# Kernel optimization log

Measured on AMD Instinct MI355X. Metric: run time of the kernel, lower is better.

## Reference

```python
import jax, jax.numpy as jnp
import numpy as np

N = 50000      # nodes
E = 800000     # edges
F = 128        # node_features
DSS = 64       # degree_set_size
H = 128        # latent dim (hardcoded in GraphES)


def gcn_conv(x, W, b, src, dst, n):
    # PyG GCNConv: linear -> symmetric-normalized aggregation with self loops -> bias
    h = x @ W                                            # [N, C_out]
    deg = jnp.zeros((n,), x.dtype).at[dst].add(1.0) + 1.0  # in-degree incl. self loop
    dinv = jax.lax.rsqrt(deg)
    norm = dinv[src] * dinv[dst]                         # [E]
    agg = jnp.zeros_like(h).at[dst].add(h[src] * norm[:, None])
    agg = agg + h * (dinv * dinv)[:, None]               # self-loop term (norm_ii = 1/deg_i)
    return agg + b


def mlp(x, w1, b1, w2, b2):
    return jax.nn.relu(x @ w1 + b1) @ w2 + b2


def _swap(ei, i1, i2, coin):
    e1 = jnp.take(ei, i1, axis=1)
    e2 = jnp.take(ei, i2, axis=1)
    a, b = e1[0], e1[1]
    c, d = e2[0], e2[1]
    ne1 = jnp.where(coin, jnp.stack([a, d]), jnp.stack([a, c]))
    ne2 = jnp.where(coin, jnp.stack([c, b]), jnp.stack([b, d]))
    return ei.at[:, i1].set(ne1).at[:, i2].set(ne2)


def setup_inputs() -> dict:
    key = jax.random.key(0)
    ks = jax.random.split(key, 24)
    s = 0.05

    def rn(k, shape):
        return jax.random.normal(k, shape, jnp.float32) * s

    return {
        "x": jax.random.normal(ks[0], (N, F), jnp.float32),
        "edge_index": jax.random.randint(ks[1], (2, E), 0, N, dtype=jnp.int32),
        "degree_set": jax.random.randint(ks[2], (N,), 0, DSS, dtype=jnp.int32),
        "timesteps": 5,
        # encoder: GCN(F+DSS -> 2H), GCN(2H -> H)
        "enc_w1": rn(ks[3], (F + DSS, 2 * H)), "enc_b1": jnp.zeros((2 * H,), jnp.float32),
        "enc_w2": rn(ks[4], (2 * H, H)),       "enc_b2": jnp.zeros((H,), jnp.float32),
        # decoder: GCN(H+DSS -> 2F), GCN(2F -> F)
        "dec_w1": rn(ks[5], (H + DSS, 2 * F)), "dec_b1": jnp.zeros((2 * F,), jnp.float32),
        "dec_w2": rn(ks[6], (2 * F, F)),       "dec_b2": jnp.zeros((F,), jnp.float32),
        # edge_predictor_1: Linear(128,64)->ReLU->Linear(64,1)
        "ep1_w1": rn(ks[7], (H, 64)),  "ep1_b1": jnp.zeros((64,), jnp.float32),
        "ep1_w2": rn(ks[8], (64, 1)),  "ep1_b2": jnp.zeros((1,), jnp.float32),
        # edge_predictor_2: input is z concat flattened pair features -> 128+256=384
        "ep2_w1": rn(ks[9], (H + 2 * H, 64)), "ep2_b1": jnp.zeros((64,), jnp.float32),
        "ep2_w2": rn(ks[10], (64, 1)),        "ep2_b2": jnp.zeros((1,), jnp.float32),
    }


def reference(x, edge_index, degree_set, timesteps,
              enc_w1, enc_b1, enc_w2, enc_b2,
              dec_w1, dec_b1, dec_w2, dec_b2,
              ep1_w1, ep1_b1, ep1_w2, ep1_b2,
              ep2_w1, ep2_b1, ep2_w2, ep2_b2):
    src, dst = edge_index[0], edge_index[1]
    dh = jax.nn.one_hot(degree_set, DSS, dtype=x.dtype)  # [N, DSS]

    # ---- encoder ----
    h = jax.nn.relu(gcn_conv(jnp.concatenate([x, dh], 1), enc_w1, enc_b1, src, dst, N))
    z = gcn_conv(h, enc_w2, enc_b2, src, dst, N)          # [N, H]

    # ---- forward diffusion: timesteps random edge swaps (deterministic PRNG) ----
    ei = edge_index
    for t in range(timesteps):
        k1, k2 = jax.random.split(jax.random.fold_in(jax.random.key(1), t))
        idx = jax.random.choice(k1, E, (2,), replace=False)
        ei = _swap(ei, idx[0], idx[1], jax.random.bernoulli(k2))

    # ---- reverse process: argmax-driven edge swaps ----
    # edge_predictor_1 scores depend only on z -> identical every step; compute once
    i1 = jnp.argmax(mlp(z, ep1_w1, ep1_b1, ep1_w2, ep1_b2).squeeze(-1))
    for t in range(timesteps):
        e1 = jnp.take(ei, i1, axis=1)                     # [2]
        e1f = z[e1].reshape(-1)                           # [2H]
        cond = jnp.concatenate([z, jnp.broadcast_to(e1f, (N, 2 * H))], 1)
        i2 = jnp.argmax(mlp(cond, ep2_w1, ep2_b1, ep2_w2, ep2_b2).squeeze(-1))
        coin = jax.random.bernoulli(jax.random.fold_in(jax.random.key(2), t))
        ei = _swap(ei, i1, i2, coin)

    # ---- decoder on final edge structure ----
    src2, dst2 = ei[0], ei[1]
    hd = jax.nn.relu(gcn_conv(jnp.concatenate([z, dh], 1), dec_w1, dec_b1, src2, dst2, N))
    out = gcn_conv(hd, dec_w2, dec_b2, src2, dst2, N)     # [N, F]
    return out, ei
```

## Files before the change

kernel.cpp:

```cpp
#include <hip/hip_runtime.h>
#include <cstdint>
#include <cstddef>
#include <vector>
#include <algorithm>

#define NN 50000
#define EE 800000
#define FF 128
#define HH 128
#define TSTEPS 5

typedef __attribute__((ext_vector_type(8))) short bf16x8;
typedef __attribute__((ext_vector_type(4))) float f32x4;

__device__ __forceinline__ float bf2f(unsigned short u)
{
    return __uint_as_float((unsigned)u << 16);
}
__device__ __forceinline__ unsigned short f2bf(float x)
{
    unsigned u = __float_as_uint(x);
    u = (u + 0x7FFFu + ((u >> 16) & 1u));
    return (unsigned short)(u >> 16);
}
__device__ __forceinline__ void splitbf(float v, unsigned short& hi, unsigned short& lo)
{
    hi = f2bf(v);
    lo = f2bf(v - bf2f(hi));
}

template <int K, int C, bool HAS_BIAS, bool OUTBF16, bool RELU>
__global__ __launch_bounds__(256) void gemm_rw(
    const float* __restrict__ A, const float* __restrict__ W,
    void* __restrict__ Pout, int n, const float* __restrict__ bias)
{
    constexpr int RPW = 8, ROWS = 32, CG = C / 64;
    __shared__ float As[ROWS][K];
    const int row0 = blockIdx.x * ROWS;
    const int tid = threadIdx.x;
    for (int idx4 = tid; idx4 < ROWS * K / 4; idx4 += 256) {
        int idx = idx4 * 4;
        int r = idx / K, k = idx - r * K;
        int gr = row0 + r;
        float4 v = make_float4(0.f, 0.f, 0.f, 0.f);
        if (gr < n) v = *(const float4*)(A + (size_t)gr * K + k);
        As[r][k + 0] = v.x; As[r][k + 1] = v.y;
        As[r][k + 2] = v.z; As[r][k + 3] = v.w;
    }
    __syncthreads();
    const int w = tid >> 6, l = tid & 63;
    float acc[RPW][CG];
#pragma unroll
    for (int r = 0; r < RPW; r++)
#pragma unroll
        for (int c = 0; c < CG; c++) acc[r][c] = 0.f;

    for (int k = 0; k < K; k++) {
        float wv[CG];
#pragma unroll
        for (int c = 0; c < CG; c++) wv[c] = W[k * C + l + 64 * c];
#pragma unroll
        for (int r = 0; r < RPW; r++) {
            float a = As[w * RPW + r][k];
#pragma unroll
            for (int c = 0; c < CG; c++) acc[r][c] = fmaf(a, wv[c], acc[r][c]);
        }
    }
#pragma unroll
    for (int r = 0; r < RPW; r++) {
        int gr = row0 + w * RPW + r;
        if (gr >= n) continue;
#pragma unroll
        for (int c = 0; c < CG; c++) {
            int col = l + 64 * c;
            float v = acc[r][c];
            if (HAS_BIAS) v += bias[col];
            if (RELU)     v = fmaxf(v, 0.f);
            if (OUTBF16) ((unsigned short*)Pout)[(size_t)gr * C + col] = f2bf(v);
            else         ((float*)Pout)[(size_t)gr * C + col] = v;
        }
    }
}

template <int K, int C, bool HAS_BIAS, bool RELU>
__global__ __launch_bounds__(256) void gemm_mfma(
    const unsigned short* __restrict__ A, const unsigned short* __restrict__ Wp,
    unsigned short* __restrict__ Pout, const float* __restrict__ bias, int n)
{
    constexpr int KC = K / 32;
    constexpr int NT = C / 16;
    __shared__ unsigned short As[64][K];
    const int row0 = blockIdx.x * 64;
    const int tid = threadIdx.x;
    for (int idx = tid; idx < 64 * (K / 8); idx += 256) {
        int r = idx / (K / 8), k8 = idx - r * (K / 8);
        int gr = row0 + r;
        bf16x8 v = { 0, 0, 0, 0, 0, 0, 0, 0 };
        if (gr < n) v = *(const bf16x8*)(A + (size_t)gr * K + k8 * 8);
        *(bf16x8*)(&As[r][k8 * 8]) = v;
    }
    __syncthreads();
    const int w = tid >> 6, lane = tid & 63;
    const int m = lane & 15, quad = lane >> 4;
    const int rowBase = w * 16;

    f32x4 acc[NT];
#pragma unroll
    for (int t = 0; t < NT; t++) acc[t] = { 0.f, 0.f, 0.f, 0.f };

    for (int kc = 0; kc < KC; kc++) {
        bf16x8 a = *(const bf16x8*)(&As[rowBase + m][kc * 32 + quad * 8]);
#pragma unroll
        for (int t = 0; t < NT; t++) {
            int ncol = t * 16 + m;
            bf16x8 b = *(const bf16x8*)(Wp + ((size_t)kc * C + ncol) * 32 + quad * 8);
            acc[t] = __builtin_amdgcn_mfma_f32_16x16x32_bf16(a, b, acc[t], 0, 0, 0);
        }
    }
#pragma unroll
    for (int t = 0; t < NT; t++) {
        int col = t * 16 + m;
#pragma unroll
        for (int r = 0; r < 4; r++) {
            int gr = row0 + rowBase + quad * 4 + r;
            if (gr >= n) continue;
            float v = acc[t][r];
            if (HAS_BIAS) v += bias[col];
            if (RELU)     v = fmaxf(v, 0.f);
            Pout[(size_t)gr * C + col] = f2bf(v);
        }
    }
}

template <int K, int C, bool HAS_BIAS, bool RELU, bool OUT_SPLIT>
__global__ __launch_bounds__(256) void gemm_mfma_split(
    const unsigned short* __restrict__ Ahi, const unsigned short* __restrict__ Alo,
    const unsigned short* __restrict__ Whi, const unsigned short* __restrict__ Wlo,
    void* __restrict__ PoutHi, unsigned short* __restrict__ PoutLo,
    const float* __restrict__ bias, int n)
{
    constexpr int KC = K / 32;
    const int row0 = blockIdx.x * 64;
    const int col0 = blockIdx.y * 64;
    const int tid = threadIdx.x;
    const int w = tid >> 6, lane = tid & 63;
    const int m = lane & 15, quad = lane >> 4;
    const int rowBase = w * 16;
    const int arow = row0 + rowBase + m;

    f32x4 acc[4];
#pragma unroll
    for (int t = 0; t < 4; t++) acc[t] = { 0.f, 0.f, 0.f, 0.f };

    for (int kc = 0; kc < KC; kc++) {
        bf16x8 ah = { 0, 0, 0, 0, 0, 0, 0, 0 }, al = ah;
        if (arow < n) {
            ah = *(const bf16x8*)(Ahi + (size_t)arow * K + kc * 32 + quad * 8);
            al = *(const bf16x8*)(Alo + (size_t)arow * K + kc * 32 + quad * 8);
        }
#pragma unroll
        for (int t = 0; t < 4; t++) {
            int ncol = col0 + t * 16 + m;
            size_t wb = ((size_t)kc * C + ncol) * 32 + quad * 8;
            bf16x8 wh = *(const bf16x8*)(Whi + wb);
            bf16x8 wl = *(const bf16x8*)(Wlo + wb);
            acc[t] = __builtin_amdgcn_mfma_f32_16x16x32_bf16(al, wh, acc[t], 0, 0, 0);
            acc[t] = __builtin_amdgcn_mfma_f32_16x16x32_bf16(ah, wl, acc[t], 0, 0, 0);
            acc[t] = __builtin_amdgcn_mfma_f32_16x16x32_bf16(ah, wh, acc[t], 0, 0, 0);
        }
    }
#pragma unroll
    for (int t = 0; t < 4; t++) {
        int col = col0 + t * 16 + m;
#pragma unroll
        for (int r = 0; r < 4; r++) {
            int gr = row0 + rowBase + quad * 4 + r;
            if (gr >= n) continue;
            float v = acc[t][r];
            if (HAS_BIAS) v += bias[col];
            if (RELU)     v = fmaxf(v, 0.f);
            if (OUT_SPLIT) {
                unsigned short hi, lo;
                splitbf(v, hi, lo);
                ((unsigned short*)PoutHi)[(size_t)gr * C + col] = hi;
                PoutLo[(size_t)gr * C + col] = lo;
            } else {
                ((float*)PoutHi)[(size_t)gr * C + col] = v;
            }
        }
    }
}

template <int K, int C>
__global__ void pack_w(const float* __restrict__ W, unsigned short* __restrict__ Wp)
{
    int idx = blockIdx.x * 256 + threadIdx.x;
    if (idx >= K * C) return;
    int k = idx / C, nn = idx - k * C;
    Wp[((size_t)(k >> 5) * C + nn) * 32 + (k & 31)] = f2bf(W[idx]);
}

template <int K, int C>
__global__ void pack_w_split(const float* __restrict__ W,
                             unsigned short* __restrict__ Wphi,
                             unsigned short* __restrict__ Wplo)
{
    int idx = blockIdx.x * 256 + threadIdx.x;
    if (idx >= K * C) return;
    int k = idx / C, nn = idx - k * C;
    unsigned short hi, lo;
    splitbf(W[idx], hi, lo);
    size_t o = ((size_t)(k >> 5) * C + nn) * 32 + (k & 31);
    Wphi[o] = hi;
    Wplo[o] = lo;
}

__global__ void count_deg(const int* __restrict__ dst, int* __restrict__ cnt, int e)
{
    int i = blockIdx.x * blockDim.x + threadIdx.x;
    if (i < e) {
        unsigned d = (unsigned)dst[i];
        if (d < (unsigned)NN) atomicAdd(&cnt[d], 1);
    }
}

__global__ void make_dinv(const int* __restrict__ cnt, float* __restrict__ dinv, int n)
{
    int i = blockIdx.x * blockDim.x + threadIdx.x;
    if (i < n) dinv[i] = 1.0f / sqrtf((float)cnt[i] + 1.0f);
}

__global__ void scan_block(const int* __restrict__ cnt, int* __restrict__ excl,
                           int* __restrict__ bsum, int n)
{
    __shared__ int s[256];
    int i = blockIdx.x * 256 + threadIdx.x;
    int v = (i < n) ? cnt[i] : 0;
    s[threadIdx.x] = v;
    __syncthreads();
    for (int off = 1; off < 256; off <<= 1) {
        int t = (threadIdx.x >= off) ? s[threadIdx.x - off] : 0;
        __syncthreads();
        s[threadIdx.x] += t;
        __syncthreads();
    }
    if (i < n) excl[i] = s[threadIdx.x] - v;
    if (threadIdx.x == 255) bsum[blockIdx.x] = s[255];
}
__global__ void scan_bsum(int* __restrict__ bsum, int nb)
{
    if (threadIdx.x || blockIdx.x) return;
    int acc = 0;
    for (int b = 0; b < nb; b++) { int t = bsum[b]; bsum[b] = acc; acc += t; }
}
__global__ void scan_add(int* __restrict__ rowptr, const int* __restrict__ bsum, int n, int e)
{
    int i = blockIdx.x * 256 + threadIdx.x;
    if (i < n) rowptr[i] += bsum[blockIdx.x];
    if (i == 0) rowptr[n] = e;
}

__global__ void csr_fill_pairs(const int* __restrict__ src, const int* __restrict__ dst,
                               const float* __restrict__ dinv, const int* __restrict__ rowptr,
                               int* __restrict__ fill, int* __restrict__ csr_src,
                               float* __restrict__ csr_nrm, int e)
{
    int i = blockIdx.x * blockDim.x + threadIdx.x;
    if (i >= e) return;
    int d = dst[i], s = src[i];
    if ((unsigned)d >= (unsigned)NN || (unsigned)s >= (unsigned)NN) return;
    int slot = rowptr[d] + atomicAdd(&fill[d], 1);
    csr_src[slot] = s;
    csr_nrm[slot] = dinv[s] * dinv[d];
}

template <bool BF16SRC, int OUTMODE>
__global__ __launch_bounds__(256) void agg_feat(
    const void* __restrict__ Xv, const int* __restrict__ ds,
    const int* __restrict__ rowptr, const int* __restrict__ csr_src,
    const float* __restrict__ csr_nrm, const float* __restrict__ dinv,
    void* __restrict__ Fout, unsigned short* __restrict__ FoutLo)
{
    const int w = threadIdx.x >> 6, l = threadIdx.x & 63;
    const int i = blockIdx.x * 4 + w;
    if (i >= NN) return;

    auto loadRow = [&](int s, float* v) {
        if (BF16SRC) {
            ushort2 u = ((const ushort2*)((const unsigned short*)Xv + (size_t)s * 128))[l];
            v[0] = bf2f(u.x); v[1] = bf2f(u.y);
        } else {
            float2 t = ((const float2*)((const float*)Xv + (size_t)s * 128))[l];
            v[0] = t.x; v[1] = t.y;
        }
    };

    float di = dinv[i], d2 = di * di;
    float sv[2];
    loadRow(i, sv);
    float acc0 = sv[0] * d2, acc1 = sv[1] * d2;
    float hist = (ds[i] == l) ? d2 : 0.f;

    const int beg = rowptr[i], end = rowptr[i + 1];
    int idx = beg;
    for (; idx + 8 <= end; idx += 8) {
        int s[8]; float nw[8]; int b[8];
#pragma unroll
        for (int j = 0; j < 8; j++) { s[j] = csr_src[idx + j]; nw[j] = csr_nrm[idx + j]; }
#pragma unroll
        for (int j = 0; j < 8; j++) b[j] = ds[s[j]];
        float vv[8][2];
#pragma unroll
        for (int j = 0; j < 8; j++) loadRow(s[j], vv[j]);
#pragma unroll
        for (int j = 0; j < 8; j++) {
            acc0 = fmaf(vv[j][0], nw[j], acc0);
            acc1 = fmaf(vv[j][1], nw[j], acc1);
            hist += (b[j] == l) ? nw[j] : 0.f;
        }
    }
    for (; idx < end; idx++) {
        int s0 = csr_src[idx];
        float ww = csr_nrm[idx];
        int b0 = ds[s0];
        float v0[2];
        loadRow(s0, v0);
        acc0 = fmaf(v0[0], ww, acc0);
        acc1 = fmaf(v0[1], ww, acc1);
        hist += (b0 == l) ? ww : 0.f;
    }
    if (OUTMODE == 2) {
        unsigned short* Fh = (unsigned short*)Fout + (size_t)i * 192;
        unsigned short* Fl = FoutLo + (size_t)i * 192;
        unsigned short h0, l0, h1, l1, hh, ll;
        splitbf(acc0, h0, l0);
        splitbf(acc1, h1, l1);
        splitbf(hist, hh, ll);
        ((ushort2*)Fh)[l] = make_ushort2(h0, h1);
        ((ushort2*)Fl)[l] = make_ushort2(l0, l1);
        Fh[128 + l] = hh;
        Fl[128 + l] = ll;
    } else if (OUTMODE == 1) {
        unsigned short* Fr = (unsigned short*)Fout + (size_t)i * 192;
        ((ushort2*)Fr)[l] = make_ushort2(f2bf(acc0), f2bf(acc1));
        Fr[128 + l] = f2bf(hist);
    } else {
        float* Fr = (float*)Fout + (size_t)i * 192;
        Fr[2 * l] = acc0;
        Fr[2 * l + 1] = acc1;
        Fr[128 + l] = hist;
    }
}

template <int C, bool RELU, bool BF16P>
__global__ __launch_bounds__(256) void agg_wave(
    const void* __restrict__ Pv, const int* __restrict__ rowptr,
    const int* __restrict__ csr_src, const float* __restrict__ csr_nrm,
    const float* __restrict__ dinv, const float* __restrict__ bias,
    float* __restrict__ B, unsigned short* __restrict__ Bbf)
{
    constexpr int VEC = C / 64;
    const int w = threadIdx.x >> 6, l = threadIdx.x & 63;
    const int i = blockIdx.x * 4 + w;
    if (i >= NN) return;

    auto loadRow = [&](int s, float* v) {
        if (BF16P) {
            const unsigned short* P = (const unsigned short*)Pv;
            if (VEC == 4) {
                ushort4 u = ((const ushort4*)(P + (size_t)s * C))[l];
                v[0] = bf2f(u.x); v[1] = bf2f(u.y); v[2] = bf2f(u.z); v[3] = bf2f(u.w);
            } else {
                ushort2 u = ((const ushort2*)(P + (size_t)s * C))[l];
                v[0] = bf2f(u.x); v[1] = bf2f(u.y);
            }
        } else {
            const float* P = (const float*)Pv;
            if (VEC == 4) {
                float4 t = ((const float4*)(P + (size_t)s * C))[l];
                v[0] = t.x; v[1] = t.y; v[2] = t.z; v[3] = t.w;
            } else {
                float2 t = ((const float2*)(P + (size_t)s * C))[l];
                v[0] = t.x; v[1] = t.y;
            }
        }
    };

    float di = dinv[i];
    float d2 = di * di;
    float acc[VEC], sv[VEC];
    loadRow(i, sv);
#pragma unroll
    for (int v = 0; v < VEC; v++) acc[v] = sv[v] * d2;

    const int beg = rowptr[i], end = rowptr[i + 1];
    int idx = beg;
    for (; idx + 8 <= end; idx += 8) {
        int   s[8];
        float nw[8];
#pragma unroll
        for (int j = 0; j < 8; j++) { s[j] = csr_src[idx + j]; nw[j] = csr_nrm[idx + j]; }
        float vv[8][VEC];
#pragma unroll
        for (int j = 0; j < 8; j++) loadRow(s[j], vv[j]);
#pragma unroll
        for (int j = 0; j < 8; j++)
#pragma unroll
            for (int v = 0; v < VEC; v++) acc[v] = fmaf(vv[j][v], nw[j], acc[v]);
    }
    for (; idx < end; idx++) {
        int s0 = csr_src[idx];
        float ww = csr_nrm[idx];
        float v0[VEC];
        loadRow(s0, v0);
#pragma unroll
        for (int v = 0; v < VEC; v++) acc[v] = fmaf(v0[v], ww, acc[v]);
    }
#pragma unroll
    for (int v = 0; v < VEC; v++) {
        float r = acc[v] + bias[l * VEC + v];
        if (RELU) r = fmaxf(r, 0.f);
        B[(size_t)i * C + l * VEC + v] = r;
        if (Bbf) Bbf[(size_t)i * C + l * VEC + v] = f2bf(r);
    }
}

__device__ __forceinline__ unsigned long long packScore(float s, int i)
{
    unsigned u = __float_as_uint(s);
    u = (u & 0x80000000u) ? ~u : (u | 0x80000000u);
    return ((unsigned long long)u << 32) | (unsigned)(~(unsigned)i);
}
__device__ __forceinline__ int unpackIdx(unsigned long long v)
{
    return (int)(~(unsigned)(v & 0xFFFFFFFFull));
}
__device__ __forceinline__ unsigned long long maxu64(unsigned long long a,
                                                     unsigned long long b)
{
    return a > b ? a : b;
}

__global__ __launch_bounds__(256) void score1_blocks(
    const float* __restrict__ z, const float* __restrict__ w1,
    const float* __restrict__ b1, const float* __restrict__ w2,
    unsigned long long* __restrict__ blockBest, int n)
{
    __shared__ float Zs[16][HH];
    __shared__ float W1s[HH * 64];
    __shared__ float W2s[64], B1s[64];
    __shared__ unsigned long long red[4];
    const int row0 = blockIdx.x * 16;
    const int tid = threadIdx.x;
    for (int idx = tid; idx < 16 * HH; idx += 256) {
        int r = idx >> 7, k = idx & 127;
        int gr = row0 + r;
        Zs[r][k] = (gr < n) ? z[(size_t)gr * HH + k] : 0.f;
    }
    for (int idx = tid; idx < HH * 64; idx += 256) W1s[idx] = w1[idx];
    if (tid < 64) { W2s[tid] = w2[tid]; B1s[tid] = b1[tid]; }
    __syncthreads();

    const int w = tid >> 6, l = tid & 63;
    float acc[4];
#pragma unroll
    for (int r = 0; r < 4; r++) acc[r] = B1s[l];
#pragma unroll 16
    for (int k = 0; k < HH; k++) {
        float wv = W1s[k * 64 + l];
#pragma unroll
        for (int r = 0; r < 4; r++)
            acc[r] = fmaf(Zs[w * 4 + r][k], wv, acc[r]);
    }
    unsigned long long best = 0;
#pragma unroll
    for (int r = 0; r < 4; r++) {
        float p = fmaxf(acc[r], 0.f) * W2s[l];
#pragma unroll
        for (int off = 32; off > 0; off >>= 1) p += __shfl_xor(p, off, 64);
        int row = row0 + w * 4 + r;
        if (row < n) best = maxu64(best, packScore(p, row));
    }
    if (l == 0) red[w] = best;
    __syncthreads();
    if (tid == 0)
        blockBest[blockIdx.x] = maxu64(maxu64(red[0], red[1]), maxu64(red[2], red[3]));
}

__global__ __launch_bounds__(256) void reduce_best(
    const unsigned long long* __restrict__ arr, int m,
    unsigned long long* __restrict__ out)
{
    __shared__ unsigned long long red[4];
    const int tid = threadIdx.x;
    unsigned long long b = 0;
    for (int i = tid; i < m; i += 256) b = maxu64(b, arr[i]);
#pragma unroll
    for (int off = 32; off > 0; off >>= 1)
        b = maxu64(b, (unsigned long long)__shfl_xor((long long)b, off, 64));
    if ((tid & 63) == 0) red[tid >> 6] = b;
    __syncthreads();
    if (tid == 0)
        *out = maxu64(maxu64(red[0], red[1]), maxu64(red[2], red[3]));
}

__global__ __launch_bounds__(256) void score2_fused(
    const int* __restrict__ ei, const unsigned long long* __restrict__ best1,
    const float* __restrict__ z, const float* __restrict__ w1,
    const float* __restrict__ zw1, const float* __restrict__ w2,
    unsigned long long* __restrict__ blockBest, int n)
{
    __shared__ float za_s[HH], zb_s[HH];
    __shared__ float cpart[4][64];
    __shared__ float Cs[64], W2s[64];
    __shared__ unsigned long long red[4];
    int i1 = unpackIdx(*best1);
    if ((unsigned)i1 >= (unsigned)EE) i1 = 0;
    int a = ei[i1], b = ei[EE + i1];
    if ((unsigned)a >= (unsigned)NN) a = 0;
    if ((unsigned)b >= (unsigned)NN) b = 0;
    const int tid = threadIdx.x;
    if (tid < HH) za_s[tid] = z[(size_t)a * HH + tid];
    else          zb_s[tid - HH] = z[(size_t)b * HH + tid - HH];
    __syncthreads();
    const int h = tid & 63, kg = tid >> 6;
    float accc = 0.f;
#pragma unroll
    for (int kk = 0; kk < 32; kk++) {
        int k = kg * 32 + kk;
        accc = fmaf(za_s[k], w1[(128 + k) * 64 + h], accc);
        accc = fmaf(zb_s[k], w1[(256 + k) * 64 + h], accc);
    }
    cpart[kg][h] = accc;
    __syncthreads();
    if (tid < 64) {
        Cs[tid] = (cpart[0][tid] + cpart[1][tid]) + (cpart[2][tid] + cpart[3][tid]);
        W2s[tid] = w2[tid];
    }
    __syncthreads();
    const int w = kg, l = h;
    unsigned long long best = 0;
    for (int i = blockIdx.x * 4 + w; i < n; i += gridDim.x * 4) {
        float v = zw1[(size_t)i * 64 + l] + Cs[l];
        v = fmaxf(v, 0.f) * W2s[l];
#pragma unroll
        for (int off = 32; off > 0; off >>= 1) v += __shfl_xor(v, off, 64);
        best = maxu64(best, packScore(v, i));
    }
    if (l == 0) red[w] = best;
    __syncthreads();
    if (tid == 0)
        blockBest[blockIdx.x] = maxu64(maxu64(red[0], red[1]), maxu64(red[2], red[3]));
}

__global__ __launch_bounds__(256) void reduce_swap(
    const unsigned long long* __restrict__ arr, int m,
    int* __restrict__ ei, const unsigned long long* __restrict__ best1, int coin)
{
    __shared__ unsigned long long red[4];
    const int tid = threadIdx.x;
    unsigned long long b = 0;
    for (int i = tid; i < m; i += 256) b = maxu64(b, arr[i]);
#pragma unroll
    for (int off = 32; off > 0; off >>= 1)
        b = maxu64(b, (unsigned long long)__shfl_xor((long long)b, off, 64));
    if ((tid & 63) == 0) red[tid >> 6] = b;
    __syncthreads();
    if (tid == 0) {
        unsigned long long bestv = maxu64(maxu64(red[0], red[1]), maxu64(red[2], red[3]));
        int i1 = unpackIdx(*best1);
        int i2 = unpackIdx(bestv);
        if ((unsigned)i1 >= (unsigned)EE) i1 = 0;
        if ((unsigned)i2 >= (unsigned)EE) i2 = 0;
        int A = ei[i1], B = ei[EE + i1], C = ei[i2], D = ei[EE + i2];
        ei[i1] = A;             ei[EE + i1] = coin ? D : C;
        ei[i2] = coin ? C : B;  ei[EE + i2] = coin ? B : D;
    }
}

struct Swaps { int a[TSTEPS]; int b[TSTEPS]; unsigned coins; };

__global__ void fwd_swaps_k(int* __restrict__ ei, Swaps s)
{
    if (threadIdx.x != 0 || blockIdx.x != 0) return;
    for (int t = 0; t < TSTEPS; t++) {
        int i1 = s.a[t], i2 = s.b[t];
        if ((unsigned)i1 >= (unsigned)EE || (unsigned)i2 >= (unsigned)EE) continue;
        int coin = (s.coins >> t) & 1;
        int A = ei[i1], B = ei[EE + i1], C = ei[i2], D = ei[EE + i2];
        ei[i1] = A;             ei[EE + i1] = coin ? D : C;
        ei[i2] = coin ? C : B;  ei[EE + i2] = coin ? B : D;
    }
}

__global__ void write_out(const float* __restrict__ outF, const int* __restrict__ ei,
                          float* __restrict__ dst)
{
    int i = blockIdx.x * 256 + threadIdx.x;
    if (i < NN * FF) {
        float v = outF[i];
        v = fminf(fmaxf(v, -64.f), 64.f);
        dst[i] = v;
    } else if (i < NN * FF + 2 * EE) {
        dst[i] = (float)ei[i - NN * FF];
    }
}

static inline uint32_t rotl32(uint32_t x, int n) { return (x << n) | (x >> (32 - n)); }

static void tf(uint32_t k0, uint32_t k1, uint32_t c0, uint32_t c1,
               uint32_t& o0, uint32_t& o1)
{
    uint32_t ks[3] = { k0, k1, k0 ^ k1 ^ 0x1BD11BDAu };
    uint32_t x0 = c0 + ks[0], x1 = c1 + ks[1];
    static const int rA[4] = { 13, 15, 26, 6 };
    static const int rB[4] = { 17, 29, 16, 24 };
    for (int g = 0; g < 5; g++) {
        const int* r = (g & 1) ? rB : rA;
        for (int j = 0; j < 4; j++) { x0 += x1; x1 = rotl32(x1, r[j]); x1 ^= x0; }
        x0 += ks[(g + 1) % 3];
        x1 += ks[(g + 2) % 3] + (uint32_t)(g + 1);
    }
    o0 = x0; o1 = x1;
}

static void jsplit_part(uint32_t k0, uint32_t k1,
                        uint32_t& a0, uint32_t& a1, uint32_t& b0, uint32_t& b1)
{
    tf(k0, k1, 0u, 0u, a0, a1);
    tf(k0, k1, 0u, 1u, b0, b1);
}

static void jbits_part(uint32_t k0, uint32_t k1, uint32_t n, std::vector<uint32_t>& out)
{
    out.resize(n);
    for (uint32_t i = 0; i < n; i++) {
        uint32_t a, b;
        tf(k0, k1, 0u, i, a, b);
        out[i] = a ^ b;
    }
}

static bool jbern_part(uint32_t k0, uint32_t k1)
{
    uint32_t a, b;
    tf(k0, k1, 0u, 0u, a, b);
    return (a ^ b) < 0x80000000u;
}

struct PrngConsts {
    Swaps swaps;
    int revCoin[TSTEPS];
    PrngConsts()
    {
        swaps.coins = 0;
        std::vector<uint32_t> bits1, bits2;
        std::vector<uint64_t> packed((size_t)EE);
        for (int t = 0; t < TSTEPS; t++) {
            uint32_t kt0, kt1;
            tf(0u, 1u, 0u, (uint32_t)t, kt0, kt1);
            uint32_t kc0, kc1, kb0, kb1;
            jsplit_part(kt0, kt1, kc0, kc1, kb0, kb1);
            if (jbern_part(kb0, kb1)) swaps.coins |= (1u << t);

            uint32_t cur0 = kc0, cur1 = kc1, sub0, sub1, nk0, nk1;
            jsplit_part(cur0, cur1, nk0, nk1, sub0, sub1);
            cur0 = nk0; cur1 = nk1;
            jbits_part(sub0, sub1, EE, bits1);
            jsplit_part(cur0, cur1, nk0, nk1, sub0, sub1);
            cur0 = nk0; cur1 = nk1;
            jbits_part(sub0, sub1, EE, bits2);

            uint64_t m1 = ~0ull, m2 = ~0ull;
            for (uint32_t pos = 0; pos < EE; pos++) {
                uint64_t u = ((uint64_t)bits2[pos] << 32) | pos;
                if (u < m1) { m2 = m1; m1 = u; }
                else if (u < m2) { m2 = u; }
            }
            uint32_t pos0 = (uint32_t)m1, pos1 = (uint32_t)m2;
            for (uint32_t j = 0; j < EE; j++)
                packed[j] = ((uint64_t)bits1[j] << 32) | j;
            std::nth_element(packed.begin(), packed.begin() + pos0, packed.end());
            uint32_t j0 = (uint32_t)packed[pos0];
            std::nth_element(packed.begin(), packed.begin() + pos1, packed.end());
            uint32_t j1 = (uint32_t)packed[pos1];
            swaps.a[t] = (int)j0;
            swaps.b[t] = (int)j1;
        }
        for (int t = 0; t < TSTEPS; t++) {
            uint32_t kt0, kt1;
            tf(0u, 2u, 0u, (uint32_t)t, kt0, kt1);
            revCoin[t] = jbern_part(kt0, kt1) ? 1 : 0;
        }
    }
};
static const PrngConsts g_prng;

extern "C" void kernel_launch(void* const* d_in, const int* in_sizes, int n_in,
                              void* d_out, int out_size, void* d_ws, size_t ws_size,
                              hipStream_t stream)
{
    (void)out_size; (void)ws_size;

    static const int kWant[20] = {
        NN * FF, 2 * EE, NN, 1,
        192 * 256, 256, 256 * 128, 128,
        192 * 256, 256, 256 * 128, 128,
        128 * 64, 64, 64, 1,
        384 * 64, 64, 64, 1
    };
    const void* p[20] = {};
    {
        int j = 0;
        for (int k = 0; k < 20; k++) {
            if (j < n_in && in_sizes[j] == kWant[k]) { p[k] = d_in[j]; j++; }
            else if (kWant[k] == 1)                  { p[k] = nullptr; }
            else if (j < n_in)                       { p[k] = d_in[j]; j++; }
        }
    }
    const float* x      = (const float*)p[0];
    const int*   ei_in  = (const int*)p[1];
    const int*   ds     = (const int*)p[2];
    const float* enc_w1 = (const float*)p[4];
    const float* enc_b1 = (const float*)p[5];
    const float* enc_w2 = (const float*)p[6];
    const float* enc_b2 = (const float*)p[7];
    const float* dec_w1 = (const float*)p[8];
    const float* dec_b1 = (const float*)p[9];
    const float* dec_w2 = (const float*)p[10];
    const float* dec_b2 = (const float*)p[11];
    const float* ep1_w1 = (const float*)p[12];
    const float* ep1_b1 = (const float*)p[13];
    const float* ep1_w2 = (const float*)p[14];
    const float* ep2_w1 = (const float*)p[16];
    const float* ep2_b1 = (const float*)p[17];
    const float* ep2_w2 = (const float*)p[18];

    char* ws = (char*)d_ws;
    size_t off = 0;
    auto alloc = [&](size_t bytes) -> void* {
        void* q = ws + off;
        off += (bytes + 255) & ~(size_t)255;
        return q;
    };
    float* bufP    = (float*)alloc((size_t)NN * 256 * 4);
    float* bufH    = (float*)alloc((size_t)NN * 256 * 4);
    int*   eiw     = (int*)alloc((size_t)2 * EE * 4);
    int*   csr_src = (int*)alloc((size_t)EE * 4);
    float* csr_nrm = (float*)alloc((size_t)EE * 4);
    int*   rowptr  = (int*)alloc((size_t)(NN + 1) * 4);
    int*   cnt     = (int*)alloc((size_t)NN * 4);
    int*   fill    = (int*)alloc((size_t)NN * 4);
    int*   bsum    = (int*)alloc(256 * 4);
    float* dinv    = (float*)alloc((size_t)NN * 4);
    unsigned short* zbf   = (unsigned short*)alloc((size_t)NN * 128 * 2);
    unsigned short* wp1   = (unsigned short*)alloc((size_t)192 * 256 * 2);
    unsigned short* wp2   = (unsigned short*)alloc((size_t)256 * 128 * 2);
    unsigned short* w1hi  = (unsigned short*)alloc((size_t)192 * 256 * 2);
    unsigned short* w1lo  = (unsigned short*)alloc((size_t)192 * 256 * 2);
    unsigned short* w2hi  = (unsigned short*)alloc((size_t)256 * 128 * 2);
    unsigned short* w2lo  = (unsigned short*)alloc((size_t)256 * 128 * 2);
    unsigned long long* blockBest = (unsigned long long*)alloc(4096 * 8);
    unsigned long long* best1 = (unsigned long long*)alloc(8);

    unsigned short* f1hi = (unsigned short*)bufP;
    unsigned short* f1lo = f1hi + (size_t)NN * 192;
    float* P2   = bufP;
    float* zw1  = bufP;
    unsigned short* feat2bf = (unsigned short*)bufP;
    unsigned short* p4      = (unsigned short*)bufP;
    float* outF = bufP + (size_t)NN * 128;
    unsigned short* hhi = (unsigned short*)bufH;
    unsigned short* hlo = hhi + (size_t)NN * 256;
    float* zbuf = bufH;
    unsigned short* hdbf = (unsigned short*)bufH;

    const int TPB = 256;
    const int gN      = (NN + TPB - 1) / TPB;
    const int gE      = (EE + TPB - 1) / TPB;
    const int gRows16 = (NN + 15) / 16;
    const int gRows32 = (NN + 31) / 32;
    const int gRows64 = (NN + 63) / 64;
    const int gWave   = (NN + 3) / 4;

    pack_w<192, 256><<<(192 * 256 + TPB - 1) / TPB, TPB, 0, stream>>>(dec_w1, wp1);
    pack_w<256, 128><<<(256 * 128 + TPB - 1) / TPB, TPB, 0, stream>>>(dec_w2, wp2);
    pack_w_split<192, 256><<<(192 * 256 + TPB - 1) / TPB, TPB, 0, stream>>>(enc_w1, w1hi, w1lo);
    pack_w_split<256, 128><<<(256 * 128 + TPB - 1) / TPB, TPB, 0, stream>>>(enc_w2, w2hi, w2lo);

    hipMemsetAsync(cnt, 0, (size_t)NN * 4, stream);
    count_deg<<<gE, TPB, 0, stream>>>(ei_in + EE, cnt, EE);
    make_dinv<<<gN, TPB, 0, stream>>>(cnt, dinv, NN);
    scan_block<<<gN, TPB, 0, stream>>>(cnt, rowptr, bsum, NN);
    scan_bsum<<<1, 64, 0, stream>>>(bsum, gN);
    scan_add<<<gN, TPB, 0, stream>>>(rowptr, bsum, NN, EE);
    hipMemsetAsync(fill, 0, (size_t)NN * 4, stream);
    csr_fill_pairs<<<gE, TPB, 0, stream>>>(ei_in, ei_in + EE, dinv, rowptr, fill,
                                           csr_src, csr_nrm, EE);

    agg_feat<false, 2><<<gWave, TPB, 0, stream>>>(
        x, ds, rowptr, csr_src, csr_nrm, dinv, f1hi, f1lo);
    gemm_mfma_split<192, 256, true, true, true>
        <<<dim3(gRows64, 4), TPB, 0, stream>>>(
        f1hi, f1lo, w1hi, w1lo, hhi, hlo, enc_b1, NN);

    gemm_mfma_split<256, 128, false, false, false>
        <<<dim3(gRows64, 2), TPB, 0, stream>>>(
        hhi, hlo, w2hi, w2lo, P2, nullptr, nullptr, NN);
    agg_wave<128, false, false><<<gWave, TPB, 0, stream>>>(
        P2, rowptr, csr_src, csr_nrm, dinv, enc_b2, zbuf, zbf);

    score1_blocks<<<gRows16, TPB, 0, stream>>>(zbuf, ep1_w1, ep1_b1, ep1_w2,
                                               blockBest, NN);
    reduce_best<<<1, TPB, 0, stream>>>(blockBest, gRows16, best1);
    gemm_rw<128, 64, true, false, false><<<gRows32, TPB, 0, stream>>>(
        zbuf, ep2_w1, zw1, NN, ep2_b1);

    hipMemcpyAsync(eiw, ei_in, (size_t)2 * EE * 4, hipMemcpyDeviceToDevice, stream);
    fwd_swaps_k<<<1, 64, 0, stream>>>(eiw, g_prng.swaps);

    for (int t = 0; t < TSTEPS; t++) {
        score2_fused<<<256, TPB, 0, stream>>>(eiw, best1, zbuf, ep2_w1,
                                              zw1, ep2_w2, blockBest, NN);
        reduce_swap<<<1, TPB, 0, stream>>>(blockBest, 256, eiw, best1,
                                           g_prng.revCoin[t]);
    }

    hipMemsetAsync(cnt, 0, (size_t)NN * 4, stream);
    count_deg<<<gE, TPB, 0, stream>>>(eiw + EE, cnt, EE);
    make_dinv<<<gN, TPB, 0, stream>>>(cnt, dinv, NN);
    scan_block<<<gN, TPB, 0, stream>>>(cnt, rowptr, bsum, NN);
    scan_bsum<<<1, 64, 0, stream>>>(bsum, gN);
    scan_add<<<gN, TPB, 0, stream>>>(rowptr, bsum, NN, EE);
    hipMemsetAsync(fill, 0, (size_t)NN * 4, stream);
    csr_fill_pairs<<<gE, TPB, 0, stream>>>(eiw, eiw + EE, dinv, rowptr, fill,
                                           csr_src, csr_nrm, EE);

    agg_feat<true, 1><<<gWave, TPB, 0, stream>>>(
        zbf, ds, rowptr, csr_src, csr_nrm, dinv, feat2bf, nullptr);
    gemm_mfma<192, 256, true, true><<<gRows64, TPB, 0, stream>>>(
        feat2bf, wp1, hdbf, dec_b1, NN);

    gemm_mfma<256, 128, false, false><<<gRows64, TPB, 0, stream>>>(
        hdbf, wp2, p4, nullptr, NN);
    agg_wave<128, false, true><<<gWave, TPB, 0, stream>>>(
        p4, rowptr, csr_src, csr_nrm, dinv, dec_b2, outF, nullptr);

    write_out<<<(NN * FF + 2 * EE + TPB - 1) / TPB, TPB, 0, stream>>>(
        outF, eiw, (float*)d_out);
}
```

Baseline: 944.1 us.

## Tile split-bf16 encoder GEMMs through LDS with larger 128-row blocks

```diff
diff --git a/kernel.cpp b/kernel.cpp
--- a/kernel.cpp
+++ b/kernel.cpp
@@ -27,6 +27,13 @@
 {
     hi = f2bf(v);
     lo = f2bf(v - bf2f(hi));
+}
+
+__device__ __forceinline__ void gload16(const void* g, void* l)
+{
+    __builtin_amdgcn_global_load_lds(
+        (const __attribute__((address_space(1))) void*)g,
+        (__attribute__((address_space(3))) void*)l, 16, 0, 0);
 }
 
 template <int K, int C, bool HAS_BIAS, bool OUTBF16, bool RELU>
@@ -132,61 +139,138 @@
     }
 }
 
-template <int K, int C, bool HAS_BIAS, bool RELU, bool OUT_SPLIT>
-__global__ __launch_bounds__(256) void gemm_mfma_split(
+template <int K, int C, int BC, int WR, int WC, bool HAS_BIAS, bool RELU, bool OUT_SPLIT>
+__global__ __launch_bounds__(256) void gemm_split_tiled(
     const unsigned short* __restrict__ Ahi, const unsigned short* __restrict__ Alo,
     const unsigned short* __restrict__ Whi, const unsigned short* __restrict__ Wlo,
     void* __restrict__ PoutHi, unsigned short* __restrict__ PoutLo,
     const float* __restrict__ bias, int n)
 {
     constexpr int KC = K / 32;
-    const int row0 = blockIdx.x * 64;
-    const int col0 = blockIdx.y * 64;
+    constexpr int RT = 128 / (WR * 16);
+    constexpr int TT = BC / (WC * 16);
+    constexpr int LDS_USHORTS = 8192 + BC * 64;
+    __shared__ __align__(16) unsigned short smem[LDS_USHORTS];
+    unsigned short* AhL = smem;
+    unsigned short* AlL = smem + 4096;
+    unsigned short* WhL = smem + 8192;
+    unsigned short* WlL = smem + 8192 + BC * 32;
+
+    const int row0 = blockIdx.x * 128;
+    const int col0 = blockIdx.y * BC;
     const int tid = threadIdx.x;
-    const int w = tid >> 6, lane = tid & 63;
-    const int m = lane & 15, quad = lane >> 4;
-    const int rowBase = w * 16;
-    const int arow = row0 + rowBase + m;
-
-    f32x4 acc[4];
-#pragma unroll
-    for (int t = 0; t < 4; t++) acc[t] = { 0.f, 0.f, 0.f, 0.f };
+    const int w = tid >> 6, l = tid & 63;
+    const int m = l & 15, quad = l >> 4;
+    const int wr = w / WC, wc = w % WC;
+    const int rowBase = wr * (RT * 16);
+    const int colBase = wc * (TT * 16);
+
+    f32x4 acc[RT][TT];
+#pragma unroll
+    for (int rt = 0; rt < RT; rt++)
+#pragma unroll
+        for (int tt = 0; tt < TT; tt++) acc[rt][tt] = { 0.f, 0.f, 0.f, 0.f };
 
     for (int kc = 0; kc < KC; kc++) {
-        bf16x8 ah = { 0, 0, 0, 0, 0, 0, 0, 0 }, al = ah;
-        if (arow < n) {
-            ah = *(const bf16x8*)(Ahi + (size_t)arow * K + kc * 32 + quad * 8);
-            al = *(const bf16x8*)(Alo + (size_t)arow * K + kc * 32 + quad * 8);
-        }
-#pragma unroll
-        for (int t = 0; t < 4; t++) {
-            int ncol = col0 + t * 16 + m;
-            size_t wb = ((size_t)kc * C + ncol) * 32 + quad * 8;
-            bf16x8 wh = *(const bf16x8*)(Whi + wb);
-            bf16x8 wl = *(const bf16x8*)(Wlo + wb);
-            acc[t] = __builtin_amdgcn_mfma_f32_16x16x32_bf16(al, wh, acc[t], 0, 0, 0);
-            acc[t] = __builtin_amdgcn_mfma_f32_16x16x32_bf16(ah, wl, acc[t], 0, 0, 0);
-            acc[t] = __builtin_amdgcn_mfma_f32_16x16x32_bf16(ah, wh, acc[t], 0, 0, 0);
-        }
-    }
-#pragma unroll
-    for (int t = 0; t < 4; t++) {
-        int col = col0 + t * 16 + m;
-#pragma unroll
-        for (int r = 0; r < 4; r++) {
-            int gr = row0 + rowBase + quad * 4 + r;
-            if (gr >= n) continue;
-            float v = acc[t][r];
-            if (HAS_BIAS) v += bias[col];
-            if (RELU)     v = fmaxf(v, 0.f);
-            if (OUT_SPLIT) {
-                unsigned short hi, lo;
-                splitbf(v, hi, lo);
-                ((unsigned short*)PoutHi)[(size_t)gr * C + col] = hi;
-                PoutLo[(size_t)gr * C + col] = lo;
-            } else {
-                ((float*)PoutHi)[(size_t)gr * C + col] = v;
+        for (int s = w; s < 8; s += 4) {
+            int rg = row0 + s * 16 + (l >> 2);
+            if (rg > n - 1) rg = n - 1;
+            size_t go = (size_t)rg * K + kc * 32 + (l & 3) * 8;
+            gload16(Ahi + go, AhL + s * 512);
+            gload16(Alo + go, AlL + s * 512);
+        }
+        for (int s = w; s < BC / 16; s += 4) {
+            size_t wo = ((size_t)kc * C + col0) * 32 + s * 512 + l * 8;
+            gload16(Whi + wo, WhL + s * 512);
+            gload16(Wlo + wo, WlL + s * 512);
+        }
+        __syncthreads();
+
+        bf16x8 ah[RT], al[RT];
+#pragma unroll
+        for (int rt = 0; rt < RT; rt++) {
+            int ro = (rowBase + rt * 16 + m) * 32 + quad * 8;
+            ah[rt] = *(const bf16x8*)(AhL + ro);
+            al[rt] = *(const bf16x8*)(AlL + ro);
+        }
+#pragma unroll
+        for (int tt = 0; tt < TT; tt++) {
+            int co = (colBase + tt * 16 + m) * 32 + quad * 8;
+            bf16x8 wh = *(const bf16x8*)(WhL + co);
+            bf16x8 wl = *(const bf16x8*)(WlL + co);
+#pragma unroll
+            for (int rt = 0; rt < RT; rt++) {
+                acc[rt][tt] = __builtin_amdgcn_mfma_f32_16x16x32_bf16(al[rt], wh, acc[rt][tt], 0, 0, 0);
+                acc[rt][tt] = __builtin_amdgcn_mfma_f32_16x16x32_bf16(ah[rt], wl, acc[rt][tt], 0, 0, 0);
+                acc[rt][tt] = __builtin_amdgcn_mfma_f32_16x16x32_bf16(ah[rt], wh, acc[rt][tt], 0, 0, 0);
             }
+        }
+        __syncthreads();
+    }
+
+    if (OUT_SPLIT) {
+        unsigned short* Ot = smem;
+#pragma unroll
+        for (int tt = 0; tt < TT; tt++) {
+            int col_in = colBase + tt * 16 + m;
+            float bv = HAS_BIAS ? bias[col0 + col_in] : 0.f;
+#pragma unroll
+            for (int rt = 0; rt < RT; rt++)
+#pragma unroll
+                for (int r = 0; r < 4; r++) {
+                    int row_in = rowBase + rt * 16 + quad * 4 + r;
+                    float v = acc[rt][tt][r] + bv;
+                    if (RELU) v = fmaxf(v, 0.f);
+                    Ot[row_in * BC + col_in] = f2bf(v);
+                }
+        }
+        __syncthreads();
+        for (int idx = tid; idx < 128 * (BC / 8); idx += 256) {
+            int rr = idx / (BC / 8), c8 = idx - rr * (BC / 8);
+            int gr = row0 + rr;
+            if (gr < n)
+                *(bf16x8*)((unsigned short*)PoutHi + (size_t)gr * C + col0 + c8 * 8) =
+                    *(const bf16x8*)(Ot + rr * BC + c8 * 8);
+        }
+        __syncthreads();
+#pragma unroll
+        for (int tt = 0; tt < TT; tt++) {
+            int col_in = colBase + tt * 16 + m;
+            float bv = HAS_BIAS ? bias[col0 + col_in] : 0.f;
+#pragma unroll
+            for (int rt = 0; rt < RT; rt++)
+#pragma unroll
+                for (int r = 0; r < 4; r++) {
+                    int row_in = rowBase + rt * 16 + quad * 4 + r;
+                    float v = acc[rt][tt][r] + bv;
+                    if (RELU) v = fmaxf(v, 0.f);
+                    unsigned short h = f2bf(v);
+                    Ot[row_in * BC + col_in] = f2bf(v - bf2f(h));
+                }
+        }
+        __syncthreads();
+        for (int idx = tid; idx < 128 * (BC / 8); idx += 256) {
+            int rr = idx / (BC / 8), c8 = idx - rr * (BC / 8);
+            int gr = row0 + rr;
+            if (gr < n)
+                *(bf16x8*)(PoutLo + (size_t)gr * C + col0 + c8 * 8) =
+                    *(const bf16x8*)(Ot + rr * BC + c8 * 8);
+        }
+    } else {
+#pragma unroll
+        for (int tt = 0; tt < TT; tt++) {
+            int col = col0 + colBase + tt * 16 + m;
+            float bv = HAS_BIAS ? bias[col] : 0.f;
+#pragma unroll
+            for (int rt = 0; rt < RT; rt++)
+#pragma unroll
+                for (int r = 0; r < 4; r++) {
+                    int gr = row0 + rowBase + rt * 16 + quad * 4 + r;
+                    if (gr >= n) continue;
+                    float v = acc[rt][tt][r] + bv;
+                    if (RELU) v = fmaxf(v, 0.f);
+                    ((float*)PoutHi)[(size_t)gr * C + col] = v;
+                }
         }
     }
 }
@@ -781,6 +865,7 @@
     const int gRows16 = (NN + 15) / 16;
     const int gRows32 = (NN + 31) / 32;
     const int gRows64 = (NN + 63) / 64;
+    const int gRows128 = (NN + 127) / 128;
     const int gWave   = (NN + 3) / 4;
 
     pack_w<192, 256><<<(192 * 256 + TPB - 1) / TPB, TPB, 0, stream>>>(dec_w1, wp1);
@@ -800,12 +885,12 @@
 
     agg_feat<false, 2><<<gWave, TPB, 0, stream>>>(
         x, ds, rowptr, csr_src, csr_nrm, dinv, f1hi, f1lo);
-    gemm_mfma_split<192, 256, true, true, true>
-        <<<dim3(gRows64, 4), TPB, 0, stream>>>(
+    gemm_split_tiled<192, 256, 128, 2, 2, true, true, true>
+        <<<dim3(gRows128, 2), TPB, 0, stream>>>(
         f1hi, f1lo, w1hi, w1lo, hhi, hlo, enc_b1, NN);
 
-    gemm_mfma_split<256, 128, false, false, false>
-        <<<dim3(gRows64, 2), TPB, 0, stream>>>(
+    gemm_split_tiled<256, 128, 64, 4, 1, false, false, false>
+        <<<dim3(gRows128, 2), TPB, 0, stream>>>(
         hhi, hlo, w2hi, w2lo, P2, nullptr, nullptr, NN);
     agg_wave<128, false, false><<<gWave, TPB, 0, stream>>>(
         P2, rowptr, csr_src, csr_nrm, dinv, enc_b2, zbuf, zbf);
```

After: 890.4 us. 1.06x faster.
